# Performance work log

Measured on AMD Instinct MI355X. Metric: run time of the kernel, lower is better.

Reference implementation:

```python
import jax, jax.numpy as jnp
import numpy as np
from jax import lax

B, T, D, H, L = 16, 256, 128, 128, 4  # batch, seq, input_size, hidden, num_layers
NUM_CLASSES = 10
EPS = 1e-5


def instancenorm(x):
    # x: [B, T, C]; InstanceNorm1d normalizes over the length dim (T) per (B, C),
    # biased variance, eps=1e-5, no affine.
    m = x.mean(axis=1, keepdims=True)
    v = x.var(axis=1, keepdims=True)
    return (x - m) / jnp.sqrt(v + EPS)


def lstm_stack(x, Wih, Whh, bih, bhh):
    # x: [B, T, I]; Wih/Whh: [L, 4H, I_or_H]; bih/bhh: [L, 4H]. Gate order i,f,g,o.
    batch = x.shape[0]
    hid = Whh.shape[-1]
    out = x
    for l in range(Wih.shape[0]):
        wih, whh, b = Wih[l], Whh[l], bih[l] + bhh[l]
        h0 = jnp.zeros((batch, hid), dtype=x.dtype)
        c0 = jnp.zeros((batch, hid), dtype=x.dtype)
        xs = out.swapaxes(0, 1)  # [T, B, I]

        def step(carry, xt):
            h, c = carry
            g = xt @ wih.T + h @ whh.T + b
            i, f, gg, o = jnp.split(g, 4, axis=-1)
            c_new = jax.nn.sigmoid(f) * c + jax.nn.sigmoid(i) * jnp.tanh(gg)
            h_new = jax.nn.sigmoid(o) * jnp.tanh(c_new)
            return (h_new, c_new), h_new

        _, hs = lax.scan(step, (h0, c0), xs)
        out = hs.swapaxes(0, 1)  # [B, T, H]
    return out


def setup_inputs() -> dict:
    key = jax.random.key(0)
    ks = jax.random.split(key, 16)
    s = 1.0 / np.sqrt(H)
    u = lambda k, shape: jax.random.uniform(k, shape, jnp.float32, -s, s)
    return {
        "x": jax.random.normal(ks[0], (B, T, D), jnp.float32),
        "Wih": u(ks[1], (L, 4 * H, D)),   # input_size == hidden_size so shapes stack
        "Whh": u(ks[2], (L, 4 * H, H)),
        "bih": u(ks[3], (L, 4 * H)),
        "bhh": u(ks[4], (L, 4 * H)),
        "proj_h_w": u(ks[5], (H, H)),
        "proj_h_b": u(ks[6], (H,)),
        "proj_x_w": u(ks[7], (H, D)),
        "proj_x_b": u(ks[8], (H,)),
        "attn_w": u(ks[9], (H,)),
        "fc_w": u(ks[10], (NUM_CLASSES, H)),
        "fc_b": u(ks[11], (NUM_CLASSES,)),
    }


def reference(x, Wih, Whh, bih, bhh, proj_h_w, proj_h_b, proj_x_w, proj_x_b, attn_w, fc_w, fc_b):
    batch, seq_len, input_dim = x.shape
    # normalize(): means/stdev are detached; torch std is unbiased (ddof=1)
    means = lax.stop_gradient(x.mean(axis=(0, 1), keepdims=True))
    stdev = lax.stop_gradient(x.std(axis=(0, 1), ddof=1, keepdims=True) + EPS)
    x = (x - means) / stdev
    x = instancenorm(x)

    lstm_out = lstm_stack(x, Wih, Whh, bih, bhh)   # dropout is identity in eval
    lstm_out = instancenorm(lstm_out)

    ph = lstm_out @ proj_h_w.T + proj_h_b           # [B, T, H]
    px = x @ proj_x_w.T + proj_x_b                  # [B, T, H]
    px = instancenorm(px)

    # additive attention over expanded [B, T, D, H] (values identical across D,
    # matching the original broadcast/expand semantics)
    combined = jnp.tanh(
        jnp.broadcast_to((ph + px)[:, :, None, :], (batch, seq_len, input_dim, ph.shape[-1]))
    )
    logits = jnp.einsum("btdh,h->btd", combined, attn_w)       # [B, T, D]
    alpha = jax.nn.softmax(logits.reshape(batch, -1), axis=1)   # softmax over T*D
    attention_map = alpha.reshape(batch, seq_len, input_dim)

    # classify: context = sum over (T, D) of lstm_out_ex * alpha
    context = jnp.einsum("bth,btd->bh", ph, attention_map)      # [B, H]
    out = context @ fc_w.T + fc_b                               # [B, num_classes]
    return out, attention_map
```

## Files before the change

kernel.cpp:

```cpp
#include <hip/hip_runtime.h>
#include <math.h>
#include <cstddef>

#define B_ 16
#define T_ 256
#define D_ 128
#define H_ 128
#define L_ 4
#define G_ 512
#define NC_ 10
#define EPS_ 1e-5f
#define C_ 16
#define NCHUNK_ (T_ / C_)

#define HROW_ 144
#define HOFF(k) ((k) + (((k) >> 5) << 2))

typedef float f4v __attribute__((ext_vector_type(4)));
typedef float f2v __attribute__((ext_vector_type(2)));

#define LOAD_W8(w, base)                                                   \
    asm volatile(                                                          \
        "global_load_dwordx4 %0, %8, off\n\t"                             \
        "global_load_dwordx4 %1, %8, off offset:16\n\t"                   \
        "global_load_dwordx4 %2, %8, off offset:32\n\t"                   \
        "global_load_dwordx4 %3, %8, off offset:48\n\t"                   \
        "global_load_dwordx4 %4, %8, off offset:64\n\t"                   \
        "global_load_dwordx4 %5, %8, off offset:80\n\t"                   \
        "global_load_dwordx4 %6, %8, off offset:96\n\t"                   \
        "global_load_dwordx4 %7, %8, off offset:112\n\t"                  \
        "s_waitcnt vmcnt(0)"                                               \
        : "=&v"(w[0]), "=&v"(w[1]), "=&v"(w[2]), "=&v"(w[3]),              \
          "=&v"(w[4]), "=&v"(w[5]), "=&v"(w[6]), "=&v"(w[7])               \
        : "v"(base)                                                        \
        : "memory")

#define LOAD_PK16(w, base)                                                 \
    asm volatile(                                                          \
        "global_load_dwordx2 %0, %16, off\n\t"                            \
        "global_load_dwordx2 %1, %16, off offset:8\n\t"                   \
        "global_load_dwordx2 %2, %16, off offset:16\n\t"                  \
        "global_load_dwordx2 %3, %16, off offset:24\n\t"                  \
        "global_load_dwordx2 %4, %16, off offset:32\n\t"                  \
        "global_load_dwordx2 %5, %16, off offset:40\n\t"                  \
        "global_load_dwordx2 %6, %16, off offset:48\n\t"                  \
        "global_load_dwordx2 %7, %16, off offset:56\n\t"                  \
        "global_load_dwordx2 %8, %16, off offset:64\n\t"                  \
        "global_load_dwordx2 %9, %16, off offset:72\n\t"                  \
        "global_load_dwordx2 %10, %16, off offset:80\n\t"                 \
        "global_load_dwordx2 %11, %16, off offset:88\n\t"                 \
        "global_load_dwordx2 %12, %16, off offset:96\n\t"                 \
        "global_load_dwordx2 %13, %16, off offset:104\n\t"                \
        "global_load_dwordx2 %14, %16, off offset:112\n\t"                \
        "global_load_dwordx2 %15, %16, off offset:120\n\t"                \
        "s_waitcnt vmcnt(0)"                                               \
        : "=&v"(w[0]), "=&v"(w[1]), "=&v"(w[2]), "=&v"(w[3]),              \
          "=&v"(w[4]), "=&v"(w[5]), "=&v"(w[6]), "=&v"(w[7]),              \
          "=&v"(w[8]), "=&v"(w[9]), "=&v"(w[10]), "=&v"(w[11]),            \
          "=&v"(w[12]), "=&v"(w[13]), "=&v"(w[14]), "=&v"(w[15])           \
        : "v"(base)                                                        \
        : "memory")

#define DOT32R(dst_, warr_, hvarr_)                                        \
    {                                                                      \
        float d0_ = 0.f, d1_ = 0.f;                                        \
        _Pragma("unroll")                                                  \
        for (int j_ = 0; j_ < 8; j_++) {                                   \
            d0_ = fmaf(warr_[j_].x, hvarr_[j_].x, d0_);                    \
            d1_ = fmaf(warr_[j_].y, hvarr_[j_].y, d1_);                    \
            d0_ = fmaf(warr_[j_].z, hvarr_[j_].z, d0_);                    \
            d1_ = fmaf(warr_[j_].w, hvarr_[j_].w, d1_);                    \
        }                                                                  \
        dst_ = d0_ + d1_;                                                  \
    }

#define DOT32PK(dst_, wpk_, hpk_)                                          \
    {                                                                      \
        f2v a0_ = {0.f, 0.f}, a1_ = {0.f, 0.f};                            \
        _Pragma("unroll")                                                  \
        for (int j_ = 0; j_ < 8; j_++) {                                   \
            asm("v_pk_fma_f32 %0, %1, %2, %0"                              \
                : "+v"(a0_) : "v"(wpk_[2 * j_]), "v"(hpk_[2 * j_]));       \
            asm("v_pk_fma_f32 %0, %1, %2, %0"                              \
                : "+v"(a1_) : "v"(wpk_[2 * j_ + 1]), "v"(hpk_[2 * j_ + 1]));\
        }                                                                  \
        dst_ = (a0_[0] + a1_[0]) + (a0_[1] + a1_[1]);                      \
    }

#define LGKM_BAR_ asm volatile("s_waitcnt lgkmcnt(0)\n\ts_barrier" ::: "memory")

__device__ __forceinline__ float sigmoid_(float x) {
    x = fminf(fmaxf(x, -30.f), 30.f);
    return 1.f / (1.f + __expf(-x));
}
__device__ __forceinline__ float tanh_(float x) {
    float ax = fminf(fabsf(x), 15.f);
    float e = __expf(2.f * ax);
    float t = 1.f - 2.f / (e + 1.f);
    return copysignf(t, x);
}
__device__ __forceinline__ float qsum4_(float z) {
    int a = __builtin_amdgcn_update_dpp(0, __float_as_int(z), 0xB1, 0xF, 0xF, true);
    z += __int_as_float(a);
    int b = __builtin_amdgcn_update_dpp(0, __float_as_int(z), 0x4E, 0xF, 0xF, true);
    z += __int_as_float(b);
    return z;
}
__device__ __forceinline__ void wait_ge_(int* p, int v) {
    if (__hip_atomic_load(p, __ATOMIC_RELAXED, __HIP_MEMORY_SCOPE_AGENT) < v) {
        do { __builtin_amdgcn_s_sleep(1); }
        while (__hip_atomic_load(p, __ATOMIC_RELAXED, __HIP_MEMORY_SCOPE_AGENT) < v);
    }
    (void)__hip_atomic_load(p, __ATOMIC_ACQUIRE, __HIP_MEMORY_SCOPE_AGENT);
}
__device__ __forceinline__ void ast_(float* p, float v) {
    __hip_atomic_store(p, v, __ATOMIC_RELAXED, __HIP_MEMORY_SCOPE_AGENT);
}
__device__ __forceinline__ float ald_(const float* p) {
    return __hip_atomic_load(p, __ATOMIC_RELAXED, __HIP_MEMORY_SCOPE_AGENT);
}

#define REC_STEP(RD, WR, PI, PF, PG, PO)                                   \
    {                                                                      \
        const f2v* hb2_ = (const f2v*)(shbuf + (RD) * HROW_ + q * 36);     \
        f2v hv[16];                                                        \
        _Pragma("unroll")                                                  \
        for (int jj_ = 0; jj_ < 16; jj_++) hv[jj_] = hb2_[jj_];            \
        float zi, zf, zg, zo;                                              \
        DOT32PK(zi, w0, hv);                                               \
        DOT32PK(zf, w1, hv);                                               \
        DOT32PK(zg, w2, hv);                                               \
        DOT32PK(zo, w3, hv);                                               \
        zi = qsum4_(zi) + (PI); zf = qsum4_(zf) + (PF);                    \
        zg = qsum4_(zg) + (PG); zo = qsum4_(zo) + (PO);                    \
        float ai = sigmoid_(zi), af = sigmoid_(zf);                        \
        float ag = tanh_(zg),    ao = sigmoid_(zo);                        \
        c = fmaf(af, c, ai * ag);                                          \
        float hn = ao * tanh_(c);                                          \
        if (q == 0) {                                                      \
            shbuf[(WR) * HROW_ + HOFF(r)] = hn;                            \
            ast_(hst, hn);                                                 \
        }                                                                  \
        hst += 128;                                                        \
        LGKM_BAR_;                                                         \
    }

__global__ __attribute__((amdgpu_waves_per_eu(2, 2))) __launch_bounds__(512)
void megascan(const float* __restrict__ x,
              const float* __restrict__ Wih, const float* __restrict__ Whh,
              const float* __restrict__ bih, const float* __restrict__ bhh,
              const float* __restrict__ proj_x_w, const float* __restrict__ proj_x_b,
              const float* __restrict__ proj_h_w, const float* __restrict__ proj_h_b,
              const float* __restrict__ attn_w,
              const float* __restrict__ fc_w, const float* __restrict__ fc_b,
              float* __restrict__ mu_bd, float* __restrict__ invn,
              float* __restrict__ psumB, float* __restrict__ psqB,
              float* __restrict__ h_glob,
              float* __restrict__ ring,
              float* __restrict__ px,
              float* __restrict__ mu_px, float* __restrict__ inv_px,
              float* __restrict__ mu_ln, float* __restrict__ inv_ln,
              float* __restrict__ lsc,
              float* __restrict__ out, float* __restrict__ out_att,
              int* __restrict__ flag_h,
              int* __restrict__ flag_g,
              int* __restrict__ flag_px,
              int* __restrict__ flag_ln,
              int* __restrict__ cnt,
              int* __restrict__ flag_norm,
              int* __restrict__ cnt_s) {
    const int wg = blockIdx.x;
    const int tid = threadIdx.x;
    __shared__ __align__(16) float shbuf[16 * HROW_];
    __shared__ __align__(16) float sAs[64][32];
    __shared__ __align__(16) float sBs[32][132];
    __shared__ float sred[64][33];
    __shared__ float stmp[256], swsh[256], sctx[512];
    __shared__ float smu[128], siv[128];

    if (wg < 64) {
        const int r = tid >> 2, q = tid & 3;
        const int l = wg >> 4, b = wg & 15;
        f2v w0[16], w1[16], w2[16], w3[16];
        const float* wl = Whh + (size_t)l * G_ * 128;
        LOAD_PK16(w0, wl + ((size_t)(0 * 128 + r)) * 128 + q * 32);
        LOAD_PK16(w1, wl + ((size_t)(1 * 128 + r)) * 128 + q * 32);
        LOAD_PK16(w2, wl + ((size_t)(2 * 128 + r)) * 128 + q * 32);
        LOAD_PK16(w3, wl + ((size_t)(3 * 128 + r)) * 128 + q * 32);
        float c = 0.f;
        if (tid < HROW_) shbuf[tid] = 0.f;
        const float* rsl = ring + ((size_t)l * 16 + b) * (4 * C_ * G_);
        float* hob = h_glob + ((size_t)l * 16 + b) * T_ * 128;
        int* fg = flag_g + l * 16 + b;
        int* fh = flag_h + l * 16 + b;
        __syncthreads();

#pragma unroll 1
        for (int k = 0; k < NCHUNK_; k++) {
            if (tid == 0) wait_ge_(fg, k + 1);
            __syncthreads();
            const float* gb = rsl + (size_t)(k & 3) * C_ * G_;
            float* hst = hob + (size_t)k * C_ * 128 + r;
            float pc0 = ald_(gb + r),                pc1 = ald_(gb + 128 + r);
            float pc2 = ald_(gb + 256 + r),          pc3 = ald_(gb + 384 + r);
            float pc4 = ald_(gb + G_ + r),           pc5 = ald_(gb + G_ + 128 + r);
            float pc6 = ald_(gb + G_ + 256 + r),     pc7 = ald_(gb + G_ + 384 + r);
            float pn0 = ald_(gb + 2 * G_ + r),       pn1 = ald_(gb + 2 * G_ + 128 + r);
            float pn2 = ald_(gb + 2 * G_ + 256 + r), pn3 = ald_(gb + 2 * G_ + 384 + r);
            float pn4 = ald_(gb + 3 * G_ + r),       pn5 = ald_(gb + 3 * G_ + 128 + r);
            float pn6 = ald_(gb + 3 * G_ + 256 + r), pn7 = ald_(gb + 3 * G_ + 384 + r);
#pragma unroll 1
            for (int u = 0; u < 8; u++) {
                float nn0 = 0.f, nn1 = 0.f, nn2 = 0.f, nn3 = 0.f;
                float nn4 = 0.f, nn5 = 0.f, nn6 = 0.f, nn7 = 0.f;
                if (u < 6) {
                    const float* g2 = gb + (size_t)(2 * u + 4) * G_;
                    nn0 = ald_(g2 + r);            nn1 = ald_(g2 + 128 + r);
                    nn2 = ald_(g2 + 256 + r);      nn3 = ald_(g2 + 384 + r);
                    nn4 = ald_(g2 + G_ + r);       nn5 = ald_(g2 + G_ + 128 + r);
                    nn6 = ald_(g2 + G_ + 256 + r); nn7 = ald_(g2 + G_ + 384 + r);
                }
                REC_STEP(0, 1, pc0, pc1, pc2, pc3)
                REC_STEP(1, 0, pc4, pc5, pc6, pc7)
                pc0 = pn0; pc1 = pn1; pc2 = pn2; pc3 = pn3;
                pc4 = pn4; pc5 = pn5; pc6 = pn6; pc7 = pn7;
                pn0 = nn0; pn1 = nn1; pn2 = nn2; pn3 = nn3;
                pn4 = nn4; pn5 = nn5; pn6 = nn6; pn7 = nn7;
            }
            __syncthreads();
            if (tid == 0) __hip_atomic_store(fh, k + 1, __ATOMIC_RELEASE, __HIP_MEMORY_SCOPE_AGENT);
        }
    } else if (wg < 128) {
        const int r = tid >> 2, q = tid & 3;
        const int l = (wg - 64) >> 4, b = (wg - 64) & 15;
        f2v w0[16], w1[16], w2[16], w3[16];
        const float* wl = Wih + (size_t)l * G_ * 128;
        LOAD_PK16(w0, wl + ((size_t)(0 * 128 + r)) * 128 + q * 32);
        LOAD_PK16(w1, wl + ((size_t)(1 * 128 + r)) * 128 + q * 32);
        LOAD_PK16(w2, wl + ((size_t)(2 * 128 + r)) * 128 + q * 32);
        LOAD_PK16(w3, wl + ((size_t)(3 * 128 + r)) * 128 + q * 32);
        float bs0 = bih[l * G_ + r] + bhh[l * G_ + r];
        float bs1 = bih[l * G_ + 128 + r] + bhh[l * G_ + 128 + r];
        float bs2 = bih[l * G_ + 256 + r] + bhh[l * G_ + 256 + r];
        float bs3 = bih[l * G_ + 384 + r] + bhh[l * G_ + 384 + r];
        const float* hsrc = (l > 0) ? h_glob + ((size_t)(l - 1) * 16 + b) * T_ * 128
                                    : x + (size_t)b * T_ * 128;
        float muk = 0.f, ivk = 1.f;
        if (l == 0) {
            if (tid == 0) wait_ge_(flag_norm + b, 1);
            __syncthreads();
            muk = mu_bd[b * 128 + (tid & 127)];
            ivk = invn[b * 128 + (tid & 127)];
        }
        float* rout = ring + ((size_t)l * 16 + b) * (4 * C_ * G_);
        int* fhp = (l > 0) ? flag_h + (l - 1) * 16 + b : flag_h;
        int* fhme = flag_h + l * 16 + b;
        int* fgo = flag_g + l * 16 + b;

#pragma unroll 1
        for (int k = 0; k < NCHUNK_; k++) {
            if (tid == 0) {
                if (l > 0) wait_ge_(fhp, k + 1);
                if (k >= 4) wait_ge_(fhme, k - 3);
            }
            __syncthreads();
#pragma unroll
            for (int i = 0; i < 4; i++) {
                int idx = i * 512 + tid;
                float v;
                if (l == 0) {
                    v = hsrc[(size_t)k * C_ * 128 + idx];
                    v = (v - muk) * ivk;
                } else {
                    v = ald_(hsrc + (size_t)k * C_ * 128 + idx);
                }
                shbuf[(idx >> 7) * HROW_ + HOFF(idx & 127)] = v;
            }
            LGKM_BAR_;
#pragma unroll 4
            for (int s = 0; s < C_; s++) {
                const f2v* hb2 = (const f2v*)(shbuf + s * HROW_ + q * 36);
                f2v hv[16];
#pragma unroll
                for (int j = 0; j < 16; j++) hv[j] = hb2[j];
                float z0, z1, z2, z3;
                DOT32PK(z0, w0, hv);
                DOT32PK(z1, w1, hv);
                DOT32PK(z2, w2, hv);
                DOT32PK(z3, w3, hv);
                z0 = qsum4_(z0); z1 = qsum4_(z1);
                z2 = qsum4_(z2); z3 = qsum4_(z3);
                if (q == 0) {
                    float* ro = rout + ((size_t)(k & 3) * C_ + s) * G_;
                    ast_(ro + r, z0 + bs0);
                    ast_(ro + 128 + r, z1 + bs1);
                    ast_(ro + 256 + r, z2 + bs2);
                    ast_(ro + 384 + r, z3 + bs3);
                }
            }
            __syncthreads();
            if (tid == 0) __hip_atomic_store(fgo, k + 1, __ATOMIC_RELEASE, __HIP_MEMORY_SCOPE_AGENT);
        }
    } else if (wg < 144) {
        const int b = wg - 128;
        const int h = tid & 127, tq = tid >> 7;
        f4v w0[8], w1[8], w2[8], w3[8];
        LOAD_W8(w0, proj_x_w + (size_t)h * 128 + 0);
        LOAD_W8(w1, proj_x_w + (size_t)h * 128 + 32);
        LOAD_W8(w2, proj_x_w + (size_t)h * 128 + 64);
        LOAD_W8(w3, proj_x_w + (size_t)h * 128 + 96);
        float bsx = proj_x_b[h];
        if (tid == 0) wait_ge_(flag_norm + b, 1);
        __syncthreads();
        float muk = mu_bd[b * 128 + h], ivk = invn[b * 128 + h];
        const float* xb = x + (size_t)b * T_ * 128;
        float* pxb = px + (size_t)b * T_ * 128;
        float sacc = 0.f, qacc = 0.f;

        for (int blk = 0; blk < 16; blk++) {
            int t0 = blk * 16;
            __syncthreads();
#pragma unroll
            for (int j = 0; j < 4; j++) {
                int tt = tq * 4 + j;
                float v = xb[(size_t)(t0 + tt) * 128 + h];
                shbuf[tt * HROW_ + HOFF(h)] = (v - muk) * ivk;
            }
            __syncthreads();
#pragma unroll
            for (int j = 0; j < 4; j++) {
                int tt = tq * 4 + j;
                const float* row = shbuf + tt * HROW_;
                f4v hv[8];
                float p0, p1, p2, p3;
                const f4v* r4 = (const f4v*)(row + 0 * 36);
#pragma unroll
                for (int u = 0; u < 8; u++) hv[u] = r4[u];
                DOT32R(p0, w0, hv);
                r4 = (const f4v*)(row + 1 * 36);
#pragma unroll
                for (int u = 0; u < 8; u++) hv[u] = r4[u];
                DOT32R(p1, w1, hv);
                r4 = (const f4v*)(row + 2 * 36);
#pragma unroll
                for (int u = 0; u < 8; u++) hv[u] = r4[u];
                DOT32R(p2, w2, hv);
                r4 = (const f4v*)(row + 3 * 36);
#pragma unroll
                for (int u = 0; u < 8; u++) hv[u] = r4[u];
                DOT32R(p3, w3, hv);
                float val = (p0 + p1) + (p2 + p3) + bsx;
                ast_(pxb + (size_t)(t0 + tt) * 128 + h, val);
                sacc += val; qacc += val * val;
            }
        }
        __syncthreads();
        shbuf[tq * 128 + h] = sacc;
        shbuf[512 + tq * 128 + h] = qacc;
        __syncthreads();
        if (tq == 0) {
            float s = shbuf[h] + shbuf[128 + h] + shbuf[256 + h] + shbuf[384 + h];
            float qq = shbuf[512 + h] + shbuf[640 + h] + shbuf[768 + h] + shbuf[896 + h];
            float m = s * (1.f / T_);
            float v = qq * (1.f / T_) - m * m;
            ast_(mu_px + b * 128 + h, m);
            ast_(inv_px + b * 128 + h, rsqrtf(fmaxf(v, 0.f) + EPS_));
        }
        __syncthreads();
        if (tid == 0) __hip_atomic_store(flag_px + b, 1, __ATOMIC_RELEASE, __HIP_MEMORY_SCOPE_AGENT);
    } else if (wg < 160) {
        const int b = wg - 144;
        const int h = tid & 127, st = tid >> 7;
        const float* hsrc = h_glob + ((size_t)3 * 16 + b) * T_ * 128;
        int* f3 = flag_h + 3 * 16 + b;
        float s = 0.f, q = 0.f;
        for (int k = 0; k < NCHUNK_; k++) {
            if (tid == 0) wait_ge_(f3, k + 1);
            __syncthreads();
#pragma unroll
            for (int j = 0; j < 4; j++) {
                int tt = st * 4 + j;
                float v = ald_(hsrc + (size_t)(k * C_ + tt) * 128 + h);
                s += v; q += v * v;
            }
        }
        shbuf[st * 128 + h] = s;
        shbuf[512 + st * 128 + h] = q;
        __syncthreads();
        if (st == 0) {
            float ss = shbuf[h] + shbuf[128 + h] + shbuf[256 + h] + shbuf[384 + h];
            float qq = shbuf[512 + h] + shbuf[640 + h] + shbuf[768 + h] + shbuf[896 + h];
            float m = ss * (1.f / T_);
            float v = qq * (1.f / T_) - m * m;
            ast_(mu_ln + b * 128 + h, m);
            ast_(inv_ln + b * 128 + h, rsqrtf(fmaxf(v, 0.f) + EPS_));
        }
        __syncthreads();
        if (tid == 0) __hip_atomic_store(flag_ln + b, 1, __ATOMIC_RELEASE, __HIP_MEMORY_SCOPE_AGENT);
    } else if (wg < 224) {
        const int blk = wg - 160;
        const int b = blk >> 2, qt = blk & 3;
        const int m0 = qt * 64;
        if (tid == 0) { wait_ge_(flag_px + b, 1); wait_ge_(flag_ln + b, 1); }
        __syncthreads();
        if (tid < 128) {
            smu[tid] = mu_px[b * 128 + tid];
            siv[tid] = inv_px[b * 128 + tid];
        }
        __syncthreads();

        const float* h3b = h_glob + ((size_t)3 * 16 + b) * T_ * 128;
        float* phg = h_glob;
        const int lr = tid >> 3, lc = (tid & 7) << 2;
        const int nB = tid >> 2, k0B = (tid & 3) << 3;
        const int tm = (tid >> 5) << 2, tn = (tid & 31) << 2;
        float acc[4][4] = {};
        const float* mup = mu_ln + b * 128;
        const float* ivp = inv_ln + b * 128;
        for (int kb = 0; kb < 128; kb += 32) {
            float4 av = *(const float4*)(h3b + (size_t)(m0 + lr) * 128 + kb + lc);
            float4 m4 = *(const float4*)(mup + kb + lc);
            float4 i4 = *(const float4*)(ivp + kb + lc);
            av.x = (av.x - m4.x) * i4.x; av.y = (av.y - m4.y) * i4.y;
            av.z = (av.z - m4.z) * i4.z; av.w = (av.w - m4.w) * i4.w;
            float4 bv0 = *(const float4*)(proj_h_w + (size_t)nB * 128 + kb + k0B);
            float4 bv1 = *(const float4*)(proj_h_w + (size_t)nB * 128 + kb + k0B + 4);
            __syncthreads();
            *(float4*)&sAs[lr][lc] = av;
            sBs[k0B + 0][nB] = bv0.x; sBs[k0B + 1][nB] = bv0.y;
            sBs[k0B + 2][nB] = bv0.z; sBs[k0B + 3][nB] = bv0.w;
            sBs[k0B + 4][nB] = bv1.x; sBs[k0B + 5][nB] = bv1.y;
            sBs[k0B + 6][nB] = bv1.z; sBs[k0B + 7][nB] = bv1.w;
            __syncthreads();
#pragma unroll
            for (int k4 = 0; k4 < 8; k4++) {
                f4v a4[4];
#pragma unroll
                for (int i = 0; i < 4; i++) a4[i] = *(const f4v*)&sAs[tm + i][k4 * 4];
#pragma unroll
                for (int kk = 0; kk < 4; kk++) {
                    f4v b4 = *(const f4v*)&sBs[k4 * 4 + kk][tn];
#pragma unroll
                    for (int i = 0; i < 4; i++) {
                        acc[i][0] = fmaf(a4[i][kk], b4.x, acc[i][0]);
                        acc[i][1] = fmaf(a4[i][kk], b4.y, acc[i][1]);
                        acc[i][2] = fmaf(a4[i][kk], b4.z, acc[i][2]);
                        acc[i][3] = fmaf(a4[i][kk], b4.w, acc[i][3]);
                    }
                }
            }
        }
        float spart[4];
#pragma unroll
        for (int i = 0; i < 4; i++) {
            int t = m0 + tm + i;
            size_t prow = ((size_t)b * 256 + t) * 128;
            f4v pxv = *(const f4v*)(px + prow + tn);
            float sp = 0.f;
#pragma unroll
            for (int j = 0; j < 4; j++) {
                int col = tn + j;
                float val = acc[i][j] + proj_h_b[col];
                ast_(phg + prow + col, val);
                float inx = (pxv[j] - smu[col]) * siv[col];
                sp = fmaf(tanh_(val + inx), attn_w[col], sp);
            }
            spart[i] = sp;
        }
        __syncthreads();
#pragma unroll
        for (int i = 0; i < 4; i++) sred[tm + i][tid & 31] = spart[i];
        __syncthreads();
        if (tid < 64) {
            float s = 0.f;
#pragma unroll
            for (int j = 0; j < 32; j++) s += sred[tid][j];
            ast_(lsc + b * 256 + m0 + tid, s);
        }
        __syncthreads();
        if (tid == 0) {
            (void)__hip_atomic_fetch_add(cnt + b, 1, __ATOMIC_ACQ_REL, __HIP_MEMORY_SCOPE_AGENT);
            wait_ge_(cnt + b, 4);
        }
        __syncthreads();
        float v = 0.f;
        if (tid < 256) { v = lsc[b * 256 + tid]; stmp[tid] = v; }
        __syncthreads();
        for (int off = 128; off > 0; off >>= 1) {
            if (tid < off) stmp[tid] = fmaxf(stmp[tid], stmp[tid + off]);
            __syncthreads();
        }
        float mx = stmp[0];
        __syncthreads();
        float e = (tid < 256) ? __expf(v - mx) : 0.f;
        if (tid < 256) stmp[tid] = e;
        __syncthreads();
        for (int off = 128; off > 0; off >>= 1) {
            if (tid < off) stmp[tid] += stmp[tid + off];
            __syncthreads();
        }
        float tot = stmp[0];
        __syncthreads();
        if (tid < 256) swsh[tid] = e / tot;
        __syncthreads();
        {
            float* ob = out_att + (size_t)b * T_ * D_ + (size_t)m0 * 128;
            const float invD = 1.f / (float)D_;
            for (int i = tid; i < 64 * 128; i += 512)
                ob[i] = swsh[m0 + (i >> 7)] * invD;
        }
        if (qt == 0) {
            int h = tid & 127, st = tid >> 7;
            float a = 0.f;
            for (int tt = st * 64; tt < st * 64 + 64; tt++)
                a = fmaf(phg[((size_t)b * 256 + tt) * 128 + h], swsh[tt], a);
            sctx[st * 128 + h] = a;
            __syncthreads();
            if (tid < 128) sctx[tid] = sctx[tid] + sctx[128 + tid] + sctx[256 + tid] + sctx[384 + tid];
            __syncthreads();
            if (tid < NC_) {
                float s = fc_b[tid];
                const float* fw = fc_w + tid * 128;
                for (int k = 0; k < 128; k++) s = fmaf(sctx[k], fw[k], s);
                out[b * NC_ + tid] = s;
            }
        }
    } else {
        const int b = wg - 224;
        const int d = tid & 127, r = tid >> 7;
        const float* xb = x + (size_t)b * T_ * 128;
        float s = 0.f, q = 0.f;
        for (int t = r; t < T_; t += 4) {
            float v = xb[(size_t)t * 128 + d];
            s += v; q += v * v;
        }
        shbuf[tid] = s; shbuf[512 + tid] = q;
        __syncthreads();
        if (r == 0) {
            s = shbuf[d] + shbuf[128 + d] + shbuf[256 + d] + shbuf[384 + d];
            q = shbuf[512 + d] + shbuf[640 + d] + shbuf[768 + d] + shbuf[896 + d];
            ast_(psumB + b * 128 + d, s);
            ast_(psqB + b * 128 + d, q);
        }
        __syncthreads();
        if (tid == 0) {
            (void)__hip_atomic_fetch_add(cnt_s, 1, __ATOMIC_ACQ_REL, __HIP_MEMORY_SCOPE_AGENT);
            wait_ge_(cnt_s, 16);
        }
        __syncthreads();
        if (tid < 128) {
            float S = 0.f, Q = 0.f, sb = 0.f, qb = 0.f;
            for (int bb = 0; bb < 16; bb++) {
                float ps = psumB[bb * 128 + tid];
                float pq = psqB[bb * 128 + tid];
                S += ps; Q += pq;
                if (bb == b) { sb = ps; qb = pq; }
            }
            float n = (float)(B_ * T_);
            float m = S / n;
            float varu = (Q - n * m * m) / (n - 1.f);
            float sd = sqrtf(fmaxf(varu, 0.f)) + EPS_;
            float mu = sb * (1.f / T_);
            float varT = qb * (1.f / T_) - mu * mu;
            ast_(mu_bd + b * 128 + tid, mu);
            ast_(invn + b * 128 + tid, rsqrtf(fmaxf(varT, 0.f) + EPS_ * sd * sd));
        }
        __syncthreads();
        if (tid == 0) __hip_atomic_store(flag_norm + b, 1, __ATOMIC_RELEASE, __HIP_MEMORY_SCOPE_AGENT);
    }
}

extern "C" void kernel_launch(void* const* d_in, const int* in_sizes, int n_in,
                              void* d_out, int out_size, void* d_ws, size_t ws_size,
                              hipStream_t stream) {
    const float* x        = (const float*)d_in[0];
    const float* Wih      = (const float*)d_in[1];
    const float* Whh      = (const float*)d_in[2];
    const float* bih      = (const float*)d_in[3];
    const float* bhh      = (const float*)d_in[4];
    const float* proj_h_w = (const float*)d_in[5];
    const float* proj_h_b = (const float*)d_in[6];
    const float* proj_x_w = (const float*)d_in[7];
    const float* proj_x_b = (const float*)d_in[8];
    const float* attn_w   = (const float*)d_in[9];
    const float* fc_w     = (const float*)d_in[10];
    const float* fc_b     = (const float*)d_in[11];
    float* out = (float*)d_out;

    float* ws = (float*)d_ws;
    const size_t NTD = (size_t)B_ * T_ * D_;
    float* h_glob = ws;
    float* ring   = h_glob + 4 * NTD;
    float* px     = ring + 4 * NTD;
    float* smalls = px + NTD;
    float* psumB  = smalls;
    float* psqB   = psumB + 2048;
    float* mu_bd  = psqB + 2048;
    float* invn   = mu_bd + 2048;
    float* mu_ln  = invn + 2048;
    float* inv_ln = mu_ln + 2048;
    float* mu_px  = inv_ln + 2048;
    float* inv_px = mu_px + 2048;
    float* lsc    = inv_px + 2048;
    int*   flags  = (int*)(lsc + 4096);
    int*   flag_h   = flags;
    int*   flag_g   = flags + 64;
    int*   flag_px  = flags + 128;
    int*   flag_ln  = flags + 144;
    int*   cnt      = flags + 160;
    int*   flag_norm= flags + 176;
    int*   cnt_s    = flags + 192;

    hipMemsetAsync((void*)flags, 0, 256 * sizeof(int), stream);

    megascan<<<240, 512, 0, stream>>>(x, Wih, Whh, bih, bhh,
                                      proj_x_w, proj_x_b, proj_h_w, proj_h_b,
                                      attn_w, fc_w, fc_b,
                                      mu_bd, invn, psumB, psqB,
                                      h_glob, ring, px,
                                      mu_px, inv_px, mu_ln, inv_ln,
                                      lsc, out, out + B_ * NC_,
                                      flag_h, flag_g, flag_px, flag_ln, cnt,
                                      flag_norm, cnt_s);
}
```

Measured before the change: 457.5 us.

## Refine LSTM wavefront sync to 4-step granularity with deferred vectorized h stores

Sub-chunk handoff flags now advance every 4 timesteps instead of every 16, both from the input-projection workgroups to the recurrence workgroups and from layer to layer. The goal is to shorten pipeline fill latency across the 4-layer wavefront. Recurrence workgroups no longer use scalar per-step global h stores. Instead, 64 threads write the previous step's h from LDS as 8-byte atomic stores, and the post-chunk __syncthreads is removed. Projection results are staged in LDS and written with packed 8-byte stores. The cost is more frequent flag polling and barriers, and the release on fh relies on ordering between stores issued by different threads without a block barrier, which may be subtle.

```diff
diff --git a/kernel.cpp b/kernel.cpp
--- a/kernel.cpp
+++ b/kernel.cpp
@@ -119,9 +119,24 @@
 __device__ __forceinline__ float ald_(const float* p) {
     return __hip_atomic_load(p, __ATOMIC_RELAXED, __HIP_MEMORY_SCOPE_AGENT);
 }
-
-#define REC_STEP(RD, WR, PI, PF, PG, PO)                                   \
+__device__ __forceinline__ void ast8_(float* p, f2v v) {
+    unsigned long long u;
+    __builtin_memcpy(&u, &v, 8);
+    __hip_atomic_store((unsigned long long*)p, u, __ATOMIC_RELAXED, __HIP_MEMORY_SCOPE_AGENT);
+}
+__device__ __forceinline__ void rel_(int* p, int v) {
+    __hip_atomic_store(p, v, __ATOMIC_RELEASE, __HIP_MEMORY_SCOPE_AGENT);
+}
+
+#define REC_STEP(RD, WR, PI, PF, PG, PO, TT)                               \
     {                                                                      \
+        if (tid < 64) {                                                    \
+            int t_ = (TT);                                                 \
+            if (t_ > 0) {                                                  \
+                f2v hh_ = *(const f2v*)(shbuf + (RD) * HROW_ + HOFF(2 * tid)); \
+                ast8_(hob + (size_t)(t_ - 1) * 128 + 2 * tid, hh_);        \
+            }                                                              \
+        }                                                                  \
         const f2v* hb2_ = (const f2v*)(shbuf + (RD) * HROW_ + q * 36);     \
         f2v hv[16];                                                        \
         _Pragma("unroll")                                                  \
@@ -137,11 +152,7 @@
         float ag = tanh_(zg),    ao = sigmoid_(zo);                        \
         c = fmaf(af, c, ai * ag);                                          \
         float hn = ao * tanh_(c);                                          \
-        if (q == 0) {                                                      \
-            shbuf[(WR) * HROW_ + HOFF(r)] = hn;                            \
-            ast_(hst, hn);                                                 \
-        }                                                                  \
-        hst += 128;                                                        \
+        if (q == 0) shbuf[(WR) * HROW_ + HOFF(r)] = hn;                    \
         LGKM_BAR_;                                                         \
     }
 
@@ -172,6 +183,7 @@
     const int wg = blockIdx.x;
     const int tid = threadIdx.x;
     __shared__ __align__(16) float shbuf[16 * HROW_];
+    __shared__ __align__(16) float zq[4][512];
     __shared__ __align__(16) float sAs[64][32];
     __shared__ __align__(16) float sBs[32][132];
     __shared__ float sred[64][33];
@@ -197,10 +209,9 @@
 
 #pragma unroll 1
         for (int k = 0; k < NCHUNK_; k++) {
-            if (tid == 0) wait_ge_(fg, k + 1);
+            if (tid == 0) wait_ge_(fg, 4 * k + 1);
             __syncthreads();
             const float* gb = rsl + (size_t)(k & 3) * C_ * G_;
-            float* hst = hob + (size_t)k * C_ * 128 + r;
             float pc0 = ald_(gb + r),                pc1 = ald_(gb + 128 + r);
             float pc2 = ald_(gb + 256 + r),          pc3 = ald_(gb + 384 + r);
             float pc4 = ald_(gb + G_ + r),           pc5 = ald_(gb + G_ + 128 + r);
@@ -211,6 +222,13 @@
             float pn6 = ald_(gb + 3 * G_ + 256 + r), pn7 = ald_(gb + 3 * G_ + 384 + r);
 #pragma unroll 1
             for (int u = 0; u < 8; u++) {
+                if (tid == 0 && u < 6 && (u & 1) == 0)
+                    wait_ge_(fg, 4 * k + (u >> 1) + 2);
+                REC_STEP(0, 1, pc0, pc1, pc2, pc3, 16 * k + 2 * u)
+                if (tid == 0 && (u & 1) == 0) {
+                    int tv = (16 * k + 2 * u) >> 2;
+                    if (tv > 0) rel_(fh, tv);
+                }
                 float nn0 = 0.f, nn1 = 0.f, nn2 = 0.f, nn3 = 0.f;
                 float nn4 = 0.f, nn5 = 0.f, nn6 = 0.f, nn7 = 0.f;
                 if (u < 6) {
@@ -220,16 +238,18 @@
                     nn4 = ald_(g2 + G_ + r);       nn5 = ald_(g2 + G_ + 128 + r);
                     nn6 = ald_(g2 + G_ + 256 + r); nn7 = ald_(g2 + G_ + 384 + r);
                 }
-                REC_STEP(0, 1, pc0, pc1, pc2, pc3)
-                REC_STEP(1, 0, pc4, pc5, pc6, pc7)
+                REC_STEP(1, 0, pc4, pc5, pc6, pc7, 16 * k + 2 * u + 1)
                 pc0 = pn0; pc1 = pn1; pc2 = pn2; pc3 = pn3;
                 pc4 = pn4; pc5 = pn5; pc6 = pn6; pc7 = pn7;
                 pn0 = nn0; pn1 = nn1; pn2 = nn2; pn3 = nn3;
                 pn4 = nn4; pn5 = nn5; pn6 = nn6; pn7 = nn7;
             }
-            __syncthreads();
-            if (tid == 0) __hip_atomic_store(fh, k + 1, __ATOMIC_RELEASE, __HIP_MEMORY_SCOPE_AGENT);
-        }
+        }
+        if (tid < 64) {
+            f2v hh = *(const f2v*)(shbuf + 0 * HROW_ + HOFF(2 * tid));
+            ast8_(hob + (size_t)255 * 128 + 2 * tid, hh);
+        }
+        if (tid == 0) rel_(fh, 64);
     } else if (wg < 128) {
         const int r = tid >> 2, q = tid & 3;
         const int l = (wg - 64) >> 4, b = (wg - 64) & 15;
@@ -245,12 +265,13 @@
         float bs3 = bih[l * G_ + 384 + r] + bhh[l * G_ + 384 + r];
         const float* hsrc = (l > 0) ? h_glob + ((size_t)(l - 1) * 16 + b) * T_ * 128
                                     : x + (size_t)b * T_ * 128;
+        const int row = tid >> 7, col = tid & 127;
         float muk = 0.f, ivk = 1.f;
         if (l == 0) {
             if (tid == 0) wait_ge_(flag_norm + b, 1);
             __syncthreads();
-            muk = mu_bd[b * 128 + (tid & 127)];
-            ivk = invn[b * 128 + (tid & 127)];
+            muk = mu_bd[b * 128 + col];
+            ivk = invn[b * 128 + col];
         }
         float* rout = ring + ((size_t)l * 16 + b) * (4 * C_ * G_);
         int* fhp = (l > 0) ? flag_h + (l - 1) * 16 + b : flag_h;
@@ -259,47 +280,51 @@
 
 #pragma unroll 1
         for (int k = 0; k < NCHUNK_; k++) {
-            if (tid == 0) {
-                if (l > 0) wait_ge_(fhp, k + 1);
-                if (k >= 4) wait_ge_(fhme, k - 3);
-            }
-            __syncthreads();
-#pragma unroll
-            for (int i = 0; i < 4; i++) {
-                int idx = i * 512 + tid;
-                float v;
-                if (l == 0) {
-                    v = hsrc[(size_t)k * C_ * 128 + idx];
-                    v = (v - muk) * ivk;
-                } else {
-                    v = ald_(hsrc + (size_t)k * C_ * 128 + idx);
+#pragma unroll 1
+            for (int qq = 0; qq < 4; qq++) {
+                if (tid == 0) {
+                    if (qq == 0 && k >= 4) wait_ge_(fhme, 4 * (k - 3));
+                    if (l > 0) wait_ge_(fhp, 4 * k + qq + 1);
                 }
-                shbuf[(idx >> 7) * HROW_ + HOFF(idx & 127)] = v;
-            }
-            LGKM_BAR_;
-#pragma unroll 4
-            for (int s = 0; s < C_; s++) {
-                const f2v* hb2 = (const f2v*)(shbuf + s * HROW_ + q * 36);
-                f2v hv[16];
-#pragma unroll
-                for (int j = 0; j < 16; j++) hv[j] = hb2[j];
-                float z0, z1, z2, z3;
-                DOT32PK(z0, w0, hv);
-                DOT32PK(z1, w1, hv);
-                DOT32PK(z2, w2, hv);
-                DOT32PK(z3, w3, hv);
-                z0 = qsum4_(z0); z1 = qsum4_(z1);
-                z2 = qsum4_(z2); z3 = qsum4_(z3);
-                if (q == 0) {
-                    float* ro = rout + ((size_t)(k & 3) * C_ + s) * G_;
-                    ast_(ro + r, z0 + bs0);
-                    ast_(ro + 128 + r, z1 + bs1);
-                    ast_(ro + 256 + r, z2 + bs2);
-                    ast_(ro + 384 + r, z3 + bs3);
+                __syncthreads();
+                {
+                    int t = k * C_ + qq * 4 + row;
+                    float v;
+                    if (l == 0) v = (hsrc[(size_t)t * 128 + col] - muk) * ivk;
+                    else        v = ald_(hsrc + (size_t)t * 128 + col);
+                    shbuf[((qq & 1) * 4 + row) * HROW_ + HOFF(col)] = v;
                 }
-            }
-            __syncthreads();
-            if (tid == 0) __hip_atomic_store(fgo, k + 1, __ATOMIC_RELEASE, __HIP_MEMORY_SCOPE_AGENT);
+                LGKM_BAR_;
+#pragma unroll
+                for (int s2 = 0; s2 < 4; s2++) {
+                    const f2v* hb2 = (const f2v*)(shbuf + ((qq & 1) * 4 + s2) * HROW_ + q * 36);
+                    f2v hv[16];
+#pragma unroll
+                    for (int j = 0; j < 16; j++) hv[j] = hb2[j];
+                    float z0, z1, z2, z3;
+                    DOT32PK(z0, w0, hv);
+                    DOT32PK(z1, w1, hv);
+                    DOT32PK(z2, w2, hv);
+                    DOT32PK(z3, w3, hv);
+                    z0 = qsum4_(z0); z1 = qsum4_(z1);
+                    z2 = qsum4_(z2); z3 = qsum4_(z3);
+                    if (q == 0) {
+                        zq[s2][r]       = z0 + bs0;
+                        zq[s2][128 + r] = z1 + bs1;
+                        zq[s2][256 + r] = z2 + bs2;
+                        zq[s2][384 + r] = z3 + bs3;
+                    }
+                }
+                LGKM_BAR_;
+                if (tid < 64) {
+                    float* rq = rout + (size_t)(k & 3) * C_ * G_ + (size_t)qq * 4 * G_;
+                    const f2v* zf = (const f2v*)&zq[0][0];
+#pragma unroll
+                    for (int j = 0; j < 16; j++)
+                        ast8_(rq + (size_t)(j * 64 + tid) * 2, zf[j * 64 + tid]);
+                }
+                if (tid == 0) rel_(fgo, 4 * k + qq + 1);
+            }
         }
     } else if (wg < 144) {
         const int b = wg - 128;
@@ -330,22 +355,22 @@
 #pragma unroll
             for (int j = 0; j < 4; j++) {
                 int tt = tq * 4 + j;
-                const float* row = shbuf + tt * HROW_;
+                const float* rowp = shbuf + tt * HROW_;
                 f4v hv[8];
                 float p0, p1, p2, p3;
-                const f4v* r4 = (const f4v*)(row + 0 * 36);
+                const f4v* r4 = (const f4v*)(rowp + 0 * 36);
 #pragma unroll
                 for (int u = 0; u < 8; u++) hv[u] = r4[u];
                 DOT32R(p0, w0, hv);
-                r4 = (const f4v*)(row + 1 * 36);
+                r4 = (const f4v*)(rowp + 1 * 36);
 #pragma unroll
                 for (int u = 0; u < 8; u++) hv[u] = r4[u];
                 DOT32R(p1, w1, hv);
-                r4 = (const f4v*)(row + 2 * 36);
+                r4 = (const f4v*)(rowp + 2 * 36);
 #pragma unroll
                 for (int u = 0; u < 8; u++) hv[u] = r4[u];
                 DOT32R(p2, w2, hv);
-                r4 = (const f4v*)(row + 3 * 36);
+                r4 = (const f4v*)(rowp + 3 * 36);
 #pragma unroll
                 for (int u = 0; u < 8; u++) hv[u] = r4[u];
                 DOT32R(p3, w3, hv);
@@ -367,25 +392,21 @@
             ast_(inv_px + b * 128 + h, rsqrtf(fmaxf(v, 0.f) + EPS_));
         }
         __syncthreads();
-        if (tid == 0) __hip_atomic_store(flag_px + b, 1, __ATOMIC_RELEASE, __HIP_MEMORY_SCOPE_AGENT);
+        if (tid == 0) rel_(flag_px + b, 1);
     } else if (wg < 160) {
         const int b = wg - 144;
         const int h = tid & 127, st = tid >> 7;
         const float* hsrc = h_glob + ((size_t)3 * 16 + b) * T_ * 128;
         int* f3 = flag_h + 3 * 16 + b;
-        float s = 0.f, q = 0.f;
-        for (int k = 0; k < NCHUNK_; k++) {
-            if (tid == 0) wait_ge_(f3, k + 1);
-            __syncthreads();
-#pragma unroll
-            for (int j = 0; j < 4; j++) {
-                int tt = st * 4 + j;
-                float v = ald_(hsrc + (size_t)(k * C_ + tt) * 128 + h);
-                s += v; q += v * v;
-            }
+        float s = 0.f, qv = 0.f;
+        for (int v = 0; v < 64; v++) {
+            if (tid == 0) wait_ge_(f3, v + 1);
+            __syncthreads();
+            float x_ = ald_(hsrc + (size_t)v * 512 + tid);
+            s += x_; qv += x_ * x_;
         }
         shbuf[st * 128 + h] = s;
-        shbuf[512 + st * 128 + h] = q;
+        shbuf[512 + st * 128 + h] = qv;
         __syncthreads();
         if (st == 0) {
             float ss = shbuf[h] + shbuf[128 + h] + shbuf[256 + h] + shbuf[384 + h];
@@ -396,7 +417,7 @@
             ast_(inv_ln + b * 128 + h, rsqrtf(fmaxf(v, 0.f) + EPS_));
         }
         __syncthreads();
-        if (tid == 0) __hip_atomic_store(flag_ln + b, 1, __ATOMIC_RELEASE, __HIP_MEMORY_SCOPE_AGENT);
+        if (tid == 0) rel_(flag_ln + b, 1);
     } else if (wg < 224) {
         const int blk = wg - 160;
         const int b = blk >> 2, qt = blk & 3;
@@ -566,7 +587,7 @@
             ast_(invn + b * 128 + tid, rsqrtf(fmaxf(varT, 0.f) + EPS_ * sd * sd));
         }
         __syncthreads();
-        if (tid == 0) __hip_atomic_store(flag_norm + b, 1, __ATOMIC_RELEASE, __HIP_MEMORY_SCOPE_AGENT);
+        if (tid == 0) rel_(flag_norm + b, 1);
     }
 }
 
```

After: 550.0 us. 1.2x slower.
